# Kernel optimization log

Measured on AMD Instinct MI355X. Metric: run time of the kernel, lower is better.

## Reference

```python
import jax, jax.numpy as jnp
import numpy as np

B, T, D, H = 2048, 2048, 3, 32  # batch, time steps, input_size, hidden_size


def setup_inputs() -> dict:
    key = jax.random.key(0)
    k0, k1, k2, k3, k4 = jax.random.split(key, 5)
    lim = 1.0 / np.sqrt(H)  # eqx.nn.GRUCell init range
    inp = jax.random.normal(k0, (B, T, D), dtype=jnp.float32)
    weight_ih = jax.random.uniform(k1, (3 * H, D), minval=-lim, maxval=lim, dtype=jnp.float32)
    weight_hh = jax.random.uniform(k2, (3 * H, H), minval=-lim, maxval=lim, dtype=jnp.float32)
    bias = jax.random.uniform(k3, (3 * H,), minval=-lim, maxval=lim, dtype=jnp.float32)
    bias_n = jax.random.uniform(k4, (H,), minval=-lim, maxval=lim, dtype=jnp.float32)
    return {"inp": inp, "weight_ih": weight_ih, "weight_hh": weight_hh,
            "bias": bias, "bias_n": bias_n}


def reference(inp, weight_ih, weight_hh, bias, bias_n):
    # inp: [B, T, D]. Faithful batched version of PinnWithGRU.__call__:
    # scan an eqx.nn.GRUCell over time from a zero hidden state, output hidden[0] per step.
    b = inp.shape[0]
    h0 = jnp.zeros((b, H), dtype=inp.dtype)
    xs = jnp.swapaxes(inp, 0, 1)  # [T, B, D]

    def step(h, x):
        ig = x @ weight_ih.T + bias      # [B, 3H] input gates (+ bias, as in eqx)
        hg = h @ weight_hh.T             # [B, 3H] hidden gates
        ir, iz, ia = jnp.split(ig, 3, axis=-1)
        hr, hz, ha = jnp.split(hg, 3, axis=-1)
        r = jax.nn.sigmoid(ir + hr)
        z = jax.nn.sigmoid(iz + hz)
        n = jnp.tanh(ia + bias_n + r * ha)
        h_new = (1.0 - z) * n + z * h
        return h_new, h_new[:, 0]        # emit first hidden unit per step

    _, out = jax.lax.scan(step, h0, xs)  # out: [T, B]
    return jnp.swapaxes(out, 0, 1)[..., None]  # [B, T, 1] (matches per-seq [T, 1])
```

## Files before the change

kernel.cpp:

```cpp
#include <hip/hip_runtime.h>


#define GRU_B 2048
#define GRU_T 2048
#define GRU_D 3
#define GRU_H 32
#define CHUNK 32

__device__ __forceinline__ float fast_sigmoid(float x) {
    float e = __expf(-x);
    return __builtin_amdgcn_rcpf(1.0f + e);
}
__device__ __forceinline__ float fast_tanh(float x) {
    float e = __expf(2.0f * x);
    return 1.0f - 2.0f * __builtin_amdgcn_rcpf(e + 1.0f);
}

__global__ __launch_bounds__(64, 1) void gru_scan_kernel(
    const float* __restrict__ inp,
    const float* __restrict__ w_ih,
    const float* __restrict__ w_hh,
    const float* __restrict__ bias,
    const float* __restrict__ bias_n,
    float* __restrict__ out)
{
    __shared__ __align__(16) float h2[80];
    __shared__ __align__(16) float x_lds[2 * CHUNK * GRU_D];

    const int lane = threadIdx.x;
    const int p    = lane & 31;
    const int hf   = lane >> 5;
    const size_t seq = 2 * (size_t)blockIdx.x + hf;

    float wr[32], wz[32], wn[32];
    {
        const float4* pr = (const float4*)(w_hh + (size_t)p * GRU_H);
        const float4* pz = (const float4*)(w_hh + (size_t)(GRU_H + p) * GRU_H);
        const float4* pn = (const float4*)(w_hh + (size_t)(2 * GRU_H + p) * GRU_H);
#pragma unroll
        for (int q = 0; q < 8; ++q) {
            float4 R = pr[q], Z = pz[q], N = pn[q];
            wr[4*q+0]=R.x; wr[4*q+1]=R.y; wr[4*q+2]=R.z; wr[4*q+3]=R.w;
            wz[4*q+0]=Z.x; wz[4*q+1]=Z.y; wz[4*q+2]=Z.z; wz[4*q+3]=Z.w;
            wn[4*q+0]=N.x; wn[4*q+1]=N.y; wn[4*q+2]=N.z; wn[4*q+3]=N.w;
        }
    }
    float wir[GRU_D], wiz[GRU_D], win[GRU_D];
#pragma unroll
    for (int d = 0; d < GRU_D; ++d) {
        wir[d] = w_ih[(size_t)p * GRU_D + d];
        wiz[d] = w_ih[(size_t)(GRU_H + p) * GRU_D + d];
        win[d] = w_ih[(size_t)(2 * GRU_H + p) * GRU_D + d];
    }
    const float bR = bias[p];
    const float bZ = bias[GRU_H + p];
    const float bN = bias[2 * GRU_H + p] + bias_n[p];

    const float* xp = inp + seq * (size_t)(GRU_T * GRU_D);
    float*       ob = out + seq * (size_t)GRU_T;

    const int hbase = 48 * hf;
    float* hw = h2 + hbase + p;
    const float4* hv = (const float4*)(h2 + hbase);

    float* xw = x_lds + 96 * hf + p;
    const float* xr = x_lds + 96 * hf;

    float h = 0.0f;
    *hw = 0.0f;

    float xa = xp[p];
    float xb2 = xp[32 + p];
    float xc2 = xp[64 + p];

    for (int c = 0; c < GRU_T / CHUNK; ++c) {
        xw[0]  = xa;
        xw[32] = xb2;
        xw[64] = xc2;
        if (c + 1 < GRU_T / CHUNK) {
            const size_t nb = (size_t)(c + 1) * (CHUNK * GRU_D);
            xa  = xp[nb + p];
            xb2 = xp[nb + 32 + p];
            xc2 = xp[nb + 64 + p];
        }

        float outreg = 0.0f;
#pragma unroll 8
        for (int s = 0; s < CHUNK; ++s) {
            const float x0 = xr[3 * s + 0];
            const float x1 = xr[3 * s + 1];
            const float x2 = xr[3 * s + 2];

            float4 hk[8];
#pragma unroll
            for (int q = 0; q < 8; ++q) hk[q] = hv[q];

            const float aR = fmaf(wir[2], x2, fmaf(wir[1], x1, fmaf(wir[0], x0, bR)));
            const float aZ = fmaf(wiz[2], x2, fmaf(wiz[1], x1, fmaf(wiz[0], x0, bZ)));
            const float aN = fmaf(win[2], x2, fmaf(win[1], x1, fmaf(win[0], x0, bN)));

            float r0=aR, r1=0.f, z0=aZ, z1=0.f, n0=0.f, n1=0.f;
#pragma unroll
            for (int q = 0; q < 8; ++q) {
                const float4 v = hk[q];
                r0 = fmaf(wr[4*q+0], v.x, r0); r1 = fmaf(wr[4*q+1], v.y, r1);
                r0 = fmaf(wr[4*q+2], v.z, r0); r1 = fmaf(wr[4*q+3], v.w, r1);
                z0 = fmaf(wz[4*q+0], v.x, z0); z1 = fmaf(wz[4*q+1], v.y, z1);
                z0 = fmaf(wz[4*q+2], v.z, z0); z1 = fmaf(wz[4*q+3], v.w, z1);
                n0 = fmaf(wn[4*q+0], v.x, n0); n1 = fmaf(wn[4*q+1], v.y, n1);
                n0 = fmaf(wn[4*q+2], v.z, n0); n1 = fmaf(wn[4*q+3], v.w, n1);
            }
            const float rg = fast_sigmoid(r0 + r1);
            const float zg = fast_sigmoid(z0 + z1);
            const float ng = fast_tanh(fmaf(rg, n0 + n1, aN));
            const float hnew = fmaf(zg, h - ng, ng);

            if (p == s - 1) outreg = hk[0].x;

            h = hnew;
            *hw = h;
        }
        {
            const float h0 = h2[hbase];
            if (p == CHUNK - 1) outreg = h0;
        }
        ob[c * CHUNK + p] = outreg;
    }
}

extern "C" void kernel_launch(void* const* d_in, const int* in_sizes, int n_in,
                              void* d_out, int out_size, void* d_ws, size_t ws_size,
                              hipStream_t stream) {
    const float* inp    = (const float*)d_in[0];
    const float* w_ih   = (const float*)d_in[1];
    const float* w_hh   = (const float*)d_in[2];
    const float* bias   = (const float*)d_in[3];
    const float* bias_n = (const float*)d_in[4];
    float* out = (float*)d_out;

    dim3 grid(GRU_B / 2);
    dim3 block(64);
    gru_scan_kernel<<<grid, block, 0, stream>>>(inp, w_ih, w_hh, bias, bias_n, out);
}
```

Before: 697.2 us.

## Broadcast hidden state via DPP row rotates and permlane32 swap instead of LDS

Remaps lanes so each sequence's 32 hidden units sit in two 16-lane rows spread across both wave halves. Each lane gathers the hidden vector through 15 DPP row-rotates plus permlane32 swaps, replacing the per-step LDS write/read round trip, with weights pre-permuted to match the rotation order. A runtime ballot probe picks the rotate direction and swap semantics and falls back to the LDS path if neither matches. Outputs are staged through LDS by a single capturing lane per sequence. The cost is many more cross-lane instructions per step and extra code size.

```diff
diff --git a/kernel.cpp b/kernel.cpp
--- a/kernel.cpp
+++ b/kernel.cpp
@@ -7,6 +7,8 @@
 #define GRU_H 32
 #define CHUNK 32
 
+typedef unsigned int uint2v __attribute__((ext_vector_type(2)));
+
 __device__ __forceinline__ float fast_sigmoid(float x) {
     float e = __expf(-x);
     return __builtin_amdgcn_rcpf(1.0f + e);
@@ -16,34 +18,39 @@
     return 1.0f - 2.0f * __builtin_amdgcn_rcpf(e + 1.0f);
 }
 
-__global__ __launch_bounds__(64, 1) void gru_scan_kernel(
-    const float* __restrict__ inp,
-    const float* __restrict__ w_ih,
-    const float* __restrict__ w_hh,
-    const float* __restrict__ bias,
-    const float* __restrict__ bias_n,
-    float* __restrict__ out)
+#define DPPF(v, CTRL) __int_as_float(__builtin_amdgcn_update_dpp( \
+    0, __float_as_int(v), (CTRL), 0xF, 0xF, false))
+
+template<bool SEL>
+__device__ __forceinline__ float swap32(float v) {
+    uint2v r = __builtin_amdgcn_permlane32_swap(
+        __float_as_uint(v), __float_as_uint(v), false, false);
+    return __uint_as_float(SEL ? r.x : r.y);
+}
+
+template<bool SEL>
+__device__ void gru_fast(
+    const float* __restrict__ xp, float* __restrict__ ob,
+    const float* __restrict__ w_ih, const float* __restrict__ w_hh,
+    const float* __restrict__ bias, const float* __restrict__ bias_n,
+    float* __restrict__ x_lds, float* __restrict__ out_stage,
+    int lane, int hf, int p, int dir)
 {
-    __shared__ __align__(16) float h2[80];
-    __shared__ __align__(16) float x_lds[2 * CHUNK * GRU_D];
-
-    const int lane = threadIdx.x;
-    const int p    = lane & 31;
-    const int hf   = lane >> 5;
-    const size_t seq = 2 * (size_t)blockIdx.x + hf;
-
-    float wr[32], wz[32], wn[32];
-    {
-        const float4* pr = (const float4*)(w_hh + (size_t)p * GRU_H);
-        const float4* pz = (const float4*)(w_hh + (size_t)(GRU_H + p) * GRU_H);
-        const float4* pn = (const float4*)(w_hh + (size_t)(2 * GRU_H + p) * GRU_H);
-#pragma unroll
-        for (int q = 0; q < 8; ++q) {
-            float4 R = pr[q], Z = pz[q], N = pn[q];
-            wr[4*q+0]=R.x; wr[4*q+1]=R.y; wr[4*q+2]=R.z; wr[4*q+3]=R.w;
-            wz[4*q+0]=Z.x; wz[4*q+1]=Z.y; wz[4*q+2]=Z.z; wz[4*q+3]=Z.w;
-            wn[4*q+0]=N.x; wn[4*q+1]=N.y; wn[4*q+2]=N.z; wn[4*q+3]=N.w;
-        }
+    const int li = lane & 15;
+    const int bb = 16 * (lane >> 5);
+
+    float wrO[16], wrX[16], wzO[16], wzX[16], wnO[16], wnX[16];
+#pragma unroll
+    for (int j = 0; j < 16; ++j) {
+        const int kk = (li + dir * j + 16) & 15;
+        const int kown = bb + kk;
+        const int koth = (bb ^ 16) + kk;
+        wrO[j] = w_hh[(size_t)p * GRU_H + kown];
+        wrX[j] = w_hh[(size_t)p * GRU_H + koth];
+        wzO[j] = w_hh[(size_t)(GRU_H + p) * GRU_H + kown];
+        wzX[j] = w_hh[(size_t)(GRU_H + p) * GRU_H + koth];
+        wnO[j] = w_hh[(size_t)(2 * GRU_H + p) * GRU_H + kown];
+        wnX[j] = w_hh[(size_t)(2 * GRU_H + p) * GRU_H + koth];
     }
     float wir[GRU_D], wiz[GRU_D], win[GRU_D];
 #pragma unroll
@@ -56,50 +63,122 @@
     const float bZ = bias[GRU_H + p];
     const float bN = bias[2 * GRU_H + p] + bias_n[p];
 
-    const float* xp = inp + seq * (size_t)(GRU_T * GRU_D);
-    float*       ob = out + seq * (size_t)GRU_T;
-
-    const int hbase = 48 * hf;
-    float* hw = h2 + hbase + p;
-    const float4* hv = (const float4*)(h2 + hbase);
-
-    float* xw = x_lds + 96 * hf + p;
+    float* xw = x_lds + 96 * hf;
     const float* xr = x_lds + 96 * hf;
+    float* osw = out_stage + 32 * hf;
+    const bool cap = (lane & 47) == 0;
 
     float h = 0.0f;
-    *hw = 0.0f;
-
-    float xa = xp[p];
-    float xb2 = xp[32 + p];
-    float xc2 = xp[64 + p];
+    float xa = xp[p], xb = xp[32 + p], xc = xp[64 + p];
 
     for (int c = 0; c < GRU_T / CHUNK; ++c) {
-        xw[0]  = xa;
-        xw[32] = xb2;
-        xw[64] = xc2;
+        xw[p] = xa; xw[32 + p] = xb; xw[64 + p] = xc;
         if (c + 1 < GRU_T / CHUNK) {
             const size_t nb = (size_t)(c + 1) * (CHUNK * GRU_D);
-            xa  = xp[nb + p];
-            xb2 = xp[nb + 32 + p];
-            xc2 = xp[nb + 64 + p];
-        }
-
-        float outreg = 0.0f;
+            xa = xp[nb + p]; xb = xp[nb + 32 + p]; xc = xp[nb + 64 + p];
+        }
 #pragma unroll 8
         for (int s = 0; s < CHUNK; ++s) {
             const float x0 = xr[3 * s + 0];
             const float x1 = xr[3 * s + 1];
             const float x2 = xr[3 * s + 2];
 
-            float4 hk[8];
-#pragma unroll
-            for (int q = 0; q < 8; ++q) hk[q] = hv[q];
+            float hr_[16];
+            hr_[0] = h;
+            hr_[1]  = DPPF(h, 0x121); hr_[2]  = DPPF(h, 0x122);
+            hr_[3]  = DPPF(h, 0x123); hr_[4]  = DPPF(h, 0x124);
+            hr_[5]  = DPPF(h, 0x125); hr_[6]  = DPPF(h, 0x126);
+            hr_[7]  = DPPF(h, 0x127); hr_[8]  = DPPF(h, 0x128);
+            hr_[9]  = DPPF(h, 0x129); hr_[10] = DPPF(h, 0x12A);
+            hr_[11] = DPPF(h, 0x12B); hr_[12] = DPPF(h, 0x12C);
+            hr_[13] = DPPF(h, 0x12D); hr_[14] = DPPF(h, 0x12E);
+            hr_[15] = DPPF(h, 0x12F);
+            float ho_[16];
+#pragma unroll
+            for (int j = 0; j < 16; ++j) ho_[j] = swap32<SEL>(hr_[j]);
 
             const float aR = fmaf(wir[2], x2, fmaf(wir[1], x1, fmaf(wir[0], x0, bR)));
             const float aZ = fmaf(wiz[2], x2, fmaf(wiz[1], x1, fmaf(wiz[0], x0, bZ)));
             const float aN = fmaf(win[2], x2, fmaf(win[1], x1, fmaf(win[0], x0, bN)));
 
-            float r0=aR, r1=0.f, z0=aZ, z1=0.f, n0=0.f, n1=0.f;
+            float r0 = aR, r1 = 0.f, z0 = aZ, z1 = 0.f, n0 = 0.f, n1 = 0.f;
+#pragma unroll
+            for (int j = 0; j < 16; ++j) {
+                r0 = fmaf(wrO[j], hr_[j], r0);
+                r1 = fmaf(wrX[j], ho_[j], r1);
+                z0 = fmaf(wzO[j], hr_[j], z0);
+                z1 = fmaf(wzX[j], ho_[j], z1);
+                n0 = fmaf(wnO[j], hr_[j], n0);
+                n1 = fmaf(wnX[j], ho_[j], n1);
+            }
+            const float rg = fast_sigmoid(r0 + r1);
+            const float zg = fast_sigmoid(z0 + z1);
+            const float ng = fast_tanh(fmaf(rg, n0 + n1, aN));
+            h = fmaf(zg, h - ng, ng);
+
+            if (cap) osw[s] = h;
+        }
+        const float ov = osw[p];
+        ob[c * CHUNK + p] = ov;
+    }
+}
+
+__device__ void gru_lds(
+    const float* __restrict__ xp, float* __restrict__ ob,
+    const float* __restrict__ w_ih, const float* __restrict__ w_hh,
+    const float* __restrict__ bias, const float* __restrict__ bias_n,
+    float* __restrict__ x_lds, float* __restrict__ out_stage,
+    float* __restrict__ h2, int lane, int hf, int p)
+{
+    float wr[32], wz[32], wn[32];
+#pragma unroll
+    for (int k = 0; k < 32; ++k) {
+        wr[k] = w_hh[(size_t)p * GRU_H + k];
+        wz[k] = w_hh[(size_t)(GRU_H + p) * GRU_H + k];
+        wn[k] = w_hh[(size_t)(2 * GRU_H + p) * GRU_H + k];
+    }
+    float wir[GRU_D], wiz[GRU_D], win[GRU_D];
+#pragma unroll
+    for (int d = 0; d < GRU_D; ++d) {
+        wir[d] = w_ih[(size_t)p * GRU_D + d];
+        wiz[d] = w_ih[(size_t)(GRU_H + p) * GRU_D + d];
+        win[d] = w_ih[(size_t)(2 * GRU_H + p) * GRU_D + d];
+    }
+    const float bR = bias[p];
+    const float bZ = bias[GRU_H + p];
+    const float bN = bias[2 * GRU_H + p] + bias_n[p];
+
+    float* hw = h2 + 48 * hf + p;
+    const float4* hv = (const float4*)(h2 + 48 * hf);
+    float* xw = x_lds + 96 * hf;
+    const float* xr = x_lds + 96 * hf;
+    float* osw = out_stage + 32 * hf;
+    const bool cap = (lane & 47) == 0;
+
+    float h = 0.0f;
+    *hw = 0.0f;
+    float xa = xp[p], xb = xp[32 + p], xc = xp[64 + p];
+
+    for (int c = 0; c < GRU_T / CHUNK; ++c) {
+        xw[p] = xa; xw[32 + p] = xb; xw[64 + p] = xc;
+        if (c + 1 < GRU_T / CHUNK) {
+            const size_t nb = (size_t)(c + 1) * (CHUNK * GRU_D);
+            xa = xp[nb + p]; xb = xp[nb + 32 + p]; xc = xp[nb + 64 + p];
+        }
+#pragma unroll 8
+        for (int s = 0; s < CHUNK; ++s) {
+            const float x0 = xr[3 * s + 0];
+            const float x1 = xr[3 * s + 1];
+            const float x2 = xr[3 * s + 2];
+            float4 hk[8];
+#pragma unroll
+            for (int q = 0; q < 8; ++q) hk[q] = hv[q];
+
+            const float aR = fmaf(wir[2], x2, fmaf(wir[1], x1, fmaf(wir[0], x0, bR)));
+            const float aZ = fmaf(wiz[2], x2, fmaf(wiz[1], x1, fmaf(wiz[0], x0, bZ)));
+            const float aN = fmaf(win[2], x2, fmaf(win[1], x1, fmaf(win[0], x0, bN)));
+
+            float r0 = aR, r1 = 0.f, z0 = aZ, z1 = 0.f, n0 = 0.f, n1 = 0.f;
 #pragma unroll
             for (int q = 0; q < 8; ++q) {
                 const float4 v = hk[q];
@@ -113,18 +192,57 @@
             const float rg = fast_sigmoid(r0 + r1);
             const float zg = fast_sigmoid(z0 + z1);
             const float ng = fast_tanh(fmaf(rg, n0 + n1, aN));
-            const float hnew = fmaf(zg, h - ng, ng);
-
-            if (p == s - 1) outreg = hk[0].x;
-
-            h = hnew;
+            h = fmaf(zg, h - ng, ng);
+            if (cap) osw[s] = h;
             *hw = h;
         }
-        {
-            const float h0 = h2[hbase];
-            if (p == CHUNK - 1) outreg = h0;
-        }
-        ob[c * CHUNK + p] = outreg;
+        const float ov = osw[p];
+        ob[c * CHUNK + p] = ov;
+    }
+}
+
+__global__ __launch_bounds__(64, 1) void gru_scan_kernel(
+    const float* __restrict__ inp, const float* __restrict__ w_ih,
+    const float* __restrict__ w_hh, const float* __restrict__ bias,
+    const float* __restrict__ bias_n, float* __restrict__ out)
+{
+    __shared__ __align__(16) float x_lds[2 * CHUNK * GRU_D];
+    __shared__ __align__(16) float out_stage[2 * CHUNK];
+    __shared__ __align__(16) float h2[80];
+
+    const int lane = threadIdx.x;
+    const int hf   = (lane >> 4) & 1;
+    const int p    = (lane & 15) + 16 * (lane >> 5);
+    const size_t seq = 2 * (size_t)blockIdx.x + hf;
+
+    const float* xp = inp + seq * (size_t)(GRU_T * GRU_D);
+    float*       ob = out + seq * (size_t)GRU_T;
+
+    int dir = 0;
+    bool swapok = false, sel = false;
+    {
+        const int li = lane & 15;
+        const int d1 = __builtin_amdgcn_update_dpp(0, li, 0x121, 0xF, 0xF, false);
+        if (__ballot(d1 == ((li + 1) & 15)) == ~0ULL)       dir = 1;
+        else if (__ballot(d1 == ((li + 15) & 15)) == ~0ULL) dir = -1;
+
+        const unsigned ul = (unsigned)lane;
+        uint2v q = __builtin_amdgcn_permlane32_swap(ul, ul, false, false);
+        const unsigned want = ul ^ 32u;
+        const bool okA = __ballot(q.x == want) == ~0ULL;
+        const bool okB = __ballot(q.y == want) == ~0ULL;
+        swapok = okA || okB;
+        sel = okA;
+    }
+
+    if (dir != 0 && swapok) {
+        if (sel) gru_fast<true >(xp, ob, w_ih, w_hh, bias, bias_n,
+                                 x_lds, out_stage, lane, hf, p, dir);
+        else     gru_fast<false>(xp, ob, w_ih, w_hh, bias, bias_n,
+                                 x_lds, out_stage, lane, hf, p, dir);
+    } else {
+        gru_lds(xp, ob, w_ih, w_hh, bias, bias_n,
+                x_lds, out_stage, h2, lane, hf, p);
     }
 }
 
```

After: 612.8 us. 12.1% less time.
